# Optimization experiments

Measured on AMD Instinct MI355X. Metric: run time of the kernel, lower is better.

## Reference

```python
import math
import jax, jax.numpy as jnp
import numpy as np

B, D, C = 2048, 512, 50000
M = math.pi / 6.0
S = 15.0
COS_M, SIN_M = math.cos(M), math.sin(M)
TH = math.cos(math.pi - M)
MM = math.sin(math.pi - M) * M
EPS = 1e-12


def setup_inputs() -> dict:
    key = jax.random.key(0)
    k1, k2, k3 = jax.random.split(key, 3)
    x = jax.random.normal(k1, (B, D), dtype=jnp.float32)
    label = jax.random.randint(k2, (B,), 0, C, dtype=jnp.int64)
    # xavier_normal_ on [C, D]: std = sqrt(2 / (C + D))
    std = math.sqrt(2.0 / (C + D))
    weight = jax.random.normal(k3, (C, D), dtype=jnp.float32) * std
    return {"x": x, "label": label, "weight": weight}


def reference(x, label, weight):
    # L2-normalize rows (F.normalize with eps clamp)
    xn = x / jnp.maximum(jnp.linalg.norm(x, axis=1, keepdims=True), EPS)
    wn = weight / jnp.maximum(jnp.linalg.norm(weight, axis=1, keepdims=True), EPS)
    cosine = xn @ wn.T  # [B, C]

    rows = jnp.arange(cosine.shape[0])
    cos_t = cosine[rows, label]  # target-class cosines [B]
    sin_t = jnp.sqrt(jnp.clip(1.0 - cos_t * cos_t, 0.0, 1.0))
    phi_t = cos_t * COS_M - sin_t * SIN_M
    # easy_margin = False branch
    phi_t = jnp.where(cos_t - TH > 0, phi_t, cos_t - MM)

    # one_hot * phi + (1 - one_hot) * cosine, then scale
    output = S * cosine.at[rows, label].set(phi_t)  # [B, C]

    logp = jax.nn.log_softmax(output, axis=1)
    loss = -jnp.mean(logp[rows, label])
    return output, loss
```

## Files before the change

kernel.cpp:

```cpp
#include <hip/hip_runtime.h>

#define B_ 2048
#define D_ 512
#define C_ 50000
#define NTILEN 391
#define NPART (NTILEN * 2)
#define PPX 49

static constexpr float S_SCALE = 15.0f;
static constexpr float COS_M_ = 0.86602540378443864676f;
static constexpr float SIN_M_ = 0.5f;
static constexpr float TH_    = -0.86602540378443864676f;
static constexpr float MM_    = 0.26179938779914943654f;

typedef unsigned short u16;
typedef __attribute__((ext_vector_type(4))) float f32x4;
typedef __attribute__((ext_vector_type(8))) short s16x8;

__device__ __forceinline__ u16 f2bf(float f) {
  unsigned u = __float_as_uint(f);
  u += 0x7fffu + ((u >> 16) & 1u);
  return (u16)(u >> 16);
}

__device__ __forceinline__ void load_lds16(const void* g, void* l) {
  __builtin_amdgcn_global_load_lds((const __attribute__((address_space(1))) void*)g,
                                   (__attribute__((address_space(3))) void*)l,
                                   16, 0, 0);
}

__global__ void rownorm_kernel(const float* __restrict__ src, u16* __restrict__ dst,
                               float* __restrict__ loss_zero) {
  const int row = blockIdx.x;
  const int tid = threadIdx.x;
  const float4* s = (const float4*)(src + (size_t)row * D_);
  float4 v = s[tid];
  float ss = v.x * v.x + v.y * v.y + v.z * v.z + v.w * v.w;
#pragma unroll
  for (int mask = 1; mask < 64; mask <<= 1) ss += __shfl_xor(ss, mask);
  __shared__ float red[2];
  if ((tid & 63) == 0) red[tid >> 6] = ss;
  __syncthreads();
  float total = red[0] + red[1];
  float inv = 1.0f / fmaxf(sqrtf(total), 1e-12f);
  ushort4 o;
  o.x = f2bf(v.x * inv); o.y = f2bf(v.y * inv);
  o.z = f2bf(v.z * inv); o.w = f2bf(v.w * inv);
  ((ushort4*)(dst + (size_t)row * D_))[tid] = o;
  if (loss_zero && row == 0 && tid == 0) *loss_zero = 0.0f;
}

__global__ __launch_bounds__(256) void aam_gemm_kernel(
    const u16* __restrict__ xn, const u16* __restrict__ wn,
    const int* __restrict__ label, float* __restrict__ out,
    float* __restrict__ partial, float* __restrict__ target) {
  __shared__ u16 sA[2][128 * 64];
  __shared__ u16 sB[2][128 * 64];

  const int bid = blockIdx.x;
  const int xcd = bid & 7;
  const int slot = bid >> 3;
  const int nt = (slot >> 4) * 8 + xcd;
  if (nt >= NTILEN) return;
  const int mt = slot & 15;
  const int m0 = mt * 128;
  const int n0 = nt * 128;

  const int tid = threadIdx.x;
  const int wave = tid >> 6;
  const int lane = tid & 63;
  const int wm = wave >> 1;
  const int wn_ = wave & 1;

  int lblr[4][4];
#pragma unroll
  for (int mf = 0; mf < 4; ++mf)
#pragma unroll
    for (int reg = 0; reg < 4; ++reg)
      lblr[mf][reg] = label[m0 + wm * 64 + mf * 16 + ((lane >> 4) << 2) + reg];

  f32x4 acc[4][4];
#pragma unroll
  for (int i = 0; i < 4; ++i)
#pragma unroll
    for (int j = 0; j < 4; ++j) {
      f32x4 z = {0.0f, 0.0f, 0.0f, 0.0f};
      acc[i][j] = z;
    }

  auto stage = [&](int kt, int b) {
    const int k0 = kt * 64;
#pragma unroll
    for (int j = 0; j < 4; ++j) {
      const int L = j * 256 + tid;
      const int m = L >> 3;
      const int cs = L & 7;
      const int kc = cs ^ (m & 7);
      load_lds16(xn + (size_t)(m0 + m) * D_ + k0 + kc * 8, &sA[b][L * 8]);
    }
#pragma unroll
    for (int j = 0; j < 4; ++j) {
      const int L = j * 256 + tid;
      const int m = L >> 3;
      const int cs = L & 7;
      const int kc = cs ^ (m & 7);
      int wr = n0 + m;
      if (wr >= C_) wr = 0;
      load_lds16(wn + (size_t)wr * D_ + k0 + kc * 8, &sB[b][L * 8]);
    }
  };

  stage(0, 0);
  int cur = 0;
  for (int kt = 0; kt < D_ / 64; ++kt) {
    if (kt + 1 < D_ / 64) {
      stage(kt + 1, cur ^ 1);
      asm volatile("s_waitcnt vmcnt(8)" ::: "memory");
    } else {
      asm volatile("s_waitcnt vmcnt(0)" ::: "memory");
    }
    __builtin_amdgcn_s_barrier();
    asm volatile("" ::: "memory");

    const u16* __restrict__ A = &sA[cur][0];
    const u16* __restrict__ Bs = &sB[cur][0];
#pragma unroll
    for (int kk = 0; kk < 2; ++kk) {
      const int chunk = kk * 4 + (lane >> 4);
      s16x8 af[4], bf[4];
#pragma unroll
      for (int mf = 0; mf < 4; ++mf) {
        const int r = wm * 64 + mf * 16 + (lane & 15);
        const int cs = chunk ^ (r & 7);
        af[mf] = *(const s16x8*)&A[r * 64 + cs * 8];
      }
#pragma unroll
      for (int nf = 0; nf < 4; ++nf) {
        const int r = wn_ * 64 + nf * 16 + (lane & 15);
        const int cs = chunk ^ (r & 7);
        bf[nf] = *(const s16x8*)&Bs[r * 64 + cs * 8];
      }
#pragma unroll
      for (int mf = 0; mf < 4; ++mf)
#pragma unroll
        for (int nf = 0; nf < 4; ++nf)
          acc[mf][nf] = __builtin_amdgcn_mfma_f32_16x16x32_bf16(af[mf], bf[nf],
                                                                acc[mf][nf], 0, 0, 0);
    }
    asm volatile("s_waitcnt lgkmcnt(0)" ::: "memory");
    __builtin_amdgcn_s_barrier();
    asm volatile("" ::: "memory");
    cur ^= 1;
  }

  const int colbase = n0 + wn_ * 64 + (lane & 15);
#pragma unroll
  for (int mf = 0; mf < 4; ++mf) {
#pragma unroll
    for (int reg = 0; reg < 4; ++reg) {
      const int row_l = wm * 64 + mf * 16 + ((lane >> 4) << 2) + reg;
      const int row_g = m0 + row_l;
      const int lbl = lblr[mf][reg];
      float v[4];
      float vmax = -INFINITY;
#pragma unroll
      for (int nf = 0; nf < 4; ++nf) {
        const int col = colbase + nf * 16;
        float cv = acc[mf][nf][reg];
        float val = S_SCALE * cv;
        if (col == lbl) {
          float st = sqrtf(fminf(fmaxf(1.0f - cv * cv, 0.0f), 1.0f));
          float phi = cv * COS_M_ - st * SIN_M_;
          float pv = (cv - TH_ > 0.0f) ? phi : (cv - MM_);
          val = S_SCALE * pv;
          target[row_g] = val;
        }
        if (col < C_) {
          __builtin_nontemporal_store(val, &out[(size_t)row_g * C_ + col]);
          v[nf] = val;
          vmax = fmaxf(vmax, val);
        } else {
          v[nf] = -INFINITY;
        }
      }
#pragma unroll
      for (int mask = 1; mask < 16; mask <<= 1)
        vmax = fmaxf(vmax, __shfl_xor(vmax, mask));
      float sev = 0.0f;
#pragma unroll
      for (int nf = 0; nf < 4; ++nf)
        if (v[nf] != -INFINITY) sev += __expf(v[nf] - vmax);
#pragma unroll
      for (int mask = 1; mask < 16; mask <<= 1) sev += __shfl_xor(sev, mask);
      if ((lane & 15) == 0) {
        float* p = partial + ((size_t)row_g * NPART + (nt * 2 + wn_)) * 2;
        p[0] = vmax;
        p[1] = sev;
      }
    }
  }
}

__global__ __launch_bounds__(256) void loss_kernel(const float* __restrict__ partial,
                                                   const float* __restrict__ target,
                                                   float* __restrict__ loss) {
  const int lane = threadIdx.x & 63;
  const int row = blockIdx.x * 4 + (threadIdx.x >> 6);
  float m = -INFINITY, l = 0.0f;
  const float2* p = (const float2*)partial + (size_t)row * NPART;
  for (int i = lane; i < NPART; i += 64) {
    float2 q = p[i];
    if (q.x > m) {
      l = l * __expf(m - q.x) + q.y;
      m = q.x;
    } else if (q.x != -INFINITY) {
      l += q.y * __expf(q.x - m);
    }
  }
#pragma unroll
  for (int mask = 1; mask < 64; mask <<= 1) {
    float m2 = __shfl_xor(m, mask);
    float l2 = __shfl_xor(l, mask);
    if (m2 > m) {
      l = l * __expf(m - m2) + l2;
      m = m2;
    } else if (m2 != -INFINITY) {
      l += l2 * __expf(m2 - m);
    }
  }
  __shared__ float sred[4];
  if (lane == 0) sred[threadIdx.x >> 6] = (m + logf(l)) - target[row];
  __syncthreads();
  if (threadIdx.x == 0)
    atomicAdd(loss, (sred[0] + sred[1] + sred[2] + sred[3]) * (1.0f / 2048.0f));
}

extern "C" void kernel_launch(void* const* d_in, const int* in_sizes, int n_in,
                              void* d_out, int out_size, void* d_ws, size_t ws_size,
                              hipStream_t stream) {
  const float* x = (const float*)d_in[0];
  const int* label = (const int*)d_in[1];
  const float* w = (const float*)d_in[2];
  float* out = (float*)d_out;
  float* loss = out + (size_t)B_ * C_;

  u16* xn = (u16*)d_ws;
  u16* wn = xn + (size_t)B_ * D_;
  float* partial = (float*)(wn + (size_t)C_ * D_);
  float* target = partial + (size_t)B_ * NPART * 2;

  rownorm_kernel<<<B_, 128, 0, stream>>>(x, xn, loss);
  rownorm_kernel<<<C_, 128, 0, stream>>>(w, wn, nullptr);
  aam_gemm_kernel<<<8 * PPX * 16, 256, 0, stream>>>(xn, wn, label, out, partial, target);
  loss_kernel<<<B_ / 4, 256, 0, stream>>>(partial, target, loss);
}
```

Baseline: 645.1 us.

## Halve GEMM K-tile to raise occupancy, precompute load addresses, merge rownorm launches

The bf16 GEMM K-tile shrinks from 64 to 32, with a matching 4-chunk XOR swizzle. This halves LDS use per block, and launch_bounds(256,5) asks for more resident waves to hide the latency of the output-store-heavy epilogue. Global load addresses are now computed once, outside the K loop. The two row-normalisation launches are merged into one grid to save a kernel launch. In exchange there are twice as many barrier and wait iterations per tile, and register pressure may rise under the tighter launch bound.

```diff
diff --git a/kernel.cpp b/kernel.cpp
--- a/kernel.cpp
+++ b/kernel.cpp
@@ -29,9 +29,14 @@
                                    16, 0, 0);
 }
 
-__global__ void rownorm_kernel(const float* __restrict__ src, u16* __restrict__ dst,
+__global__ void rownorm_kernel(const float* __restrict__ x, u16* __restrict__ xn,
+                               const float* __restrict__ w, u16* __restrict__ wn,
                                float* __restrict__ loss_zero) {
-  const int row = blockIdx.x;
+  const int br = blockIdx.x;
+  const bool isx = br < B_;
+  const int row = isx ? br : br - B_;
+  const float* src = isx ? x : w;
+  u16* dst = isx ? xn : wn;
   const int tid = threadIdx.x;
   const float4* s = (const float4*)(src + (size_t)row * D_);
   float4 v = s[tid];
@@ -47,15 +52,15 @@
   o.x = f2bf(v.x * inv); o.y = f2bf(v.y * inv);
   o.z = f2bf(v.z * inv); o.w = f2bf(v.w * inv);
   ((ushort4*)(dst + (size_t)row * D_))[tid] = o;
-  if (loss_zero && row == 0 && tid == 0) *loss_zero = 0.0f;
-}
-
-__global__ __launch_bounds__(256) void aam_gemm_kernel(
+  if (br == 0 && tid == 0) *loss_zero = 0.0f;
+}
+
+__global__ __launch_bounds__(256, 5) void aam_gemm_kernel(
     const u16* __restrict__ xn, const u16* __restrict__ wn,
     const int* __restrict__ label, float* __restrict__ out,
     float* __restrict__ partial, float* __restrict__ target) {
-  __shared__ u16 sA[2][128 * 64];
-  __shared__ u16 sB[2][128 * 64];
+  __shared__ u16 sA[2][128 * 32];
+  __shared__ u16 sB[2][128 * 32];
 
   const int bid = blockIdx.x;
   const int xcd = bid & 7;
@@ -78,6 +83,7 @@
 #pragma unroll
     for (int reg = 0; reg < 4; ++reg)
       lblr[mf][reg] = label[m0 + wm * 64 + mf * 16 + ((lane >> 4) << 2) + reg];
+  asm volatile("s_waitcnt vmcnt(0)" ::: "memory");
 
   f32x4 acc[4][4];
 #pragma unroll
@@ -88,34 +94,38 @@
       acc[i][j] = z;
     }
 
+  const u16* gA[2];
+  const u16* gB[2];
+  int ldsOff[2];
+#pragma unroll
+  for (int j = 0; j < 2; ++j) {
+    const int L = j * 256 + tid;
+    const int m = L >> 2;
+    const int cs = L & 3;
+    const int kc = cs ^ ((m >> 1) & 3);
+    ldsOff[j] = L * 8;
+    gA[j] = xn + (size_t)(m0 + m) * D_ + kc * 8;
+    int wr = n0 + m;
+    if (wr >= C_) wr = 0;
+    gB[j] = wn + (size_t)wr * D_ + kc * 8;
+  }
+
   auto stage = [&](int kt, int b) {
-    const int k0 = kt * 64;
-#pragma unroll
-    for (int j = 0; j < 4; ++j) {
-      const int L = j * 256 + tid;
-      const int m = L >> 3;
-      const int cs = L & 7;
-      const int kc = cs ^ (m & 7);
-      load_lds16(xn + (size_t)(m0 + m) * D_ + k0 + kc * 8, &sA[b][L * 8]);
-    }
-#pragma unroll
-    for (int j = 0; j < 4; ++j) {
-      const int L = j * 256 + tid;
-      const int m = L >> 3;
-      const int cs = L & 7;
-      const int kc = cs ^ (m & 7);
-      int wr = n0 + m;
-      if (wr >= C_) wr = 0;
-      load_lds16(wn + (size_t)wr * D_ + k0 + kc * 8, &sB[b][L * 8]);
-    }
+    const int k0 = kt * 32;
+#pragma unroll
+    for (int j = 0; j < 2; ++j)
+      load_lds16(gA[j] + k0, &sA[b][ldsOff[j]]);
+#pragma unroll
+    for (int j = 0; j < 2; ++j)
+      load_lds16(gB[j] + k0, &sB[b][ldsOff[j]]);
   };
 
   stage(0, 0);
   int cur = 0;
-  for (int kt = 0; kt < D_ / 64; ++kt) {
-    if (kt + 1 < D_ / 64) {
+  for (int kt = 0; kt < D_ / 32; ++kt) {
+    if (kt + 1 < D_ / 32) {
       stage(kt + 1, cur ^ 1);
-      asm volatile("s_waitcnt vmcnt(8)" ::: "memory");
+      asm volatile("s_waitcnt vmcnt(4)" ::: "memory");
     } else {
       asm volatile("s_waitcnt vmcnt(0)" ::: "memory");
     }
@@ -124,29 +134,27 @@
 
     const u16* __restrict__ A = &sA[cur][0];
     const u16* __restrict__ Bs = &sB[cur][0];
-#pragma unroll
-    for (int kk = 0; kk < 2; ++kk) {
-      const int chunk = kk * 4 + (lane >> 4);
-      s16x8 af[4], bf[4];
-#pragma unroll
-      for (int mf = 0; mf < 4; ++mf) {
-        const int r = wm * 64 + mf * 16 + (lane & 15);
-        const int cs = chunk ^ (r & 7);
-        af[mf] = *(const s16x8*)&A[r * 64 + cs * 8];
-      }
-#pragma unroll
-      for (int nf = 0; nf < 4; ++nf) {
-        const int r = wn_ * 64 + nf * 16 + (lane & 15);
-        const int cs = chunk ^ (r & 7);
-        bf[nf] = *(const s16x8*)&Bs[r * 64 + cs * 8];
-      }
-#pragma unroll
-      for (int mf = 0; mf < 4; ++mf)
-#pragma unroll
-        for (int nf = 0; nf < 4; ++nf)
-          acc[mf][nf] = __builtin_amdgcn_mfma_f32_16x16x32_bf16(af[mf], bf[nf],
-                                                                acc[mf][nf], 0, 0, 0);
-    }
+    const int chunk = lane >> 4;
+    s16x8 af[4], bf[4];
+#pragma unroll
+    for (int mf = 0; mf < 4; ++mf) {
+      const int r = wm * 64 + mf * 16 + (lane & 15);
+      const int cs = chunk ^ ((r >> 1) & 3);
+      af[mf] = *(const s16x8*)&A[r * 32 + cs * 8];
+    }
+#pragma unroll
+    for (int nf = 0; nf < 4; ++nf) {
+      const int r = wn_ * 64 + nf * 16 + (lane & 15);
+      const int cs = chunk ^ ((r >> 1) & 3);
+      bf[nf] = *(const s16x8*)&Bs[r * 32 + cs * 8];
+    }
+#pragma unroll
+    for (int mf = 0; mf < 4; ++mf)
+#pragma unroll
+      for (int nf = 0; nf < 4; ++nf)
+        acc[mf][nf] = __builtin_amdgcn_mfma_f32_16x16x32_bf16(af[mf], bf[nf],
+                                                              acc[mf][nf], 0, 0, 0);
+
     asm volatile("s_waitcnt lgkmcnt(0)" ::: "memory");
     __builtin_amdgcn_s_barrier();
     asm volatile("" ::: "memory");
@@ -249,8 +257,7 @@
   float* partial = (float*)(wn + (size_t)C_ * D_);
   float* target = partial + (size_t)B_ * NPART * 2;
 
-  rownorm_kernel<<<B_, 128, 0, stream>>>(x, xn, loss);
-  rownorm_kernel<<<C_, 128, 0, stream>>>(w, wn, nullptr);
+  rownorm_kernel<<<B_ + C_, 128, 0, stream>>>(x, xn, w, wn, loss);
   aam_gemm_kernel<<<8 * PPX * 16, 256, 0, stream>>>(xn, wn, label, out, partial, target);
   loss_kernel<<<B_ / 4, 256, 0, stream>>>(partial, target, loss);
 }
```

Measured after the change: 790.7 us. 1.23x slower.
